# Performance work log

Hardware: AMD Instinct MI355X
Metric: run time of the kernel (lower is better)

## Reference

```python
import jax, jax.numpy as jnp
import numpy as np

WS = 7           # window_size
NUM_HEADS = 4
DIM = 128
BNW = 4096       # batch * num_windows
NW = 64          # windows per image (attn_mask leading dim)
N = WS * WS      # tokens per window = 49


def make_rel_idx(ws: int) -> np.ndarray:
    coords = np.stack(np.meshgrid(np.arange(ws), np.arange(ws), indexing='ij'))  # (2, ws, ws)
    flat = coords.reshape(2, -1)                                                  # (2, N)
    rel = flat[:, :, None] - flat[:, None, :]                                     # (2, N, N)
    rel = rel.transpose(1, 2, 0).copy()
    rel[:, :, 0] += ws - 1
    rel[:, :, 1] += ws - 1
    rel[:, :, 0] *= 2 * ws - 1
    return rel.sum(-1).astype(np.int32)                                           # (N, N)


def setup_inputs() -> dict:
    key = jax.random.key(0)
    ks = jax.random.split(key, 4)
    x = jax.random.normal(ks[0], (BNW, N, DIM), dtype=jnp.float32)
    attn_mask = jnp.zeros((NW, N, N), dtype=jnp.float32)
    qkv_w = jax.random.normal(ks[1], (3 * DIM, DIM), dtype=jnp.float32) * 0.02
    qkv_b = jnp.zeros((3 * DIM,), dtype=jnp.float32)
    proj_w = jax.random.normal(ks[2], (DIM, DIM), dtype=jnp.float32) * 0.02
    proj_b = jnp.zeros((DIM,), dtype=jnp.float32)
    bias_table = jax.random.normal(ks[3], ((2 * WS - 1) ** 2, NUM_HEADS), dtype=jnp.float32) * 0.02
    rel_idx = jnp.asarray(make_rel_idx(WS))
    return {"x": x, "attn_mask": attn_mask, "qkv_w": qkv_w, "qkv_b": qkv_b,
            "proj_w": proj_w, "proj_b": proj_b, "bias_table": bias_table,
            "rel_idx": rel_idx}


def reference(x, attn_mask, qkv_w, qkv_b, proj_w, proj_b, bias_table, rel_idx):
    BnW, n, C = x.shape
    H = NUM_HEADS
    hd = C // H
    scale = hd ** -0.5
    # qkv projection: (BnW, n, 3C) -> (3, BnW, H, n, hd)
    qkv = (x @ qkv_w.T + qkv_b).reshape(BnW, n, 3, H, hd).transpose(2, 0, 3, 1, 4)
    q, k, v = qkv[0], qkv[1], qkv[2]
    attn = jnp.einsum('bhnd,bhmd->bhnm', q * scale, k)          # (BnW, H, n, n)
    bias = bias_table[rel_idx]                                   # (n, n, H)
    attn = attn + bias.transpose(2, 0, 1)[None]                  # broadcast (1, H, n, n)
    nW = attn_mask.shape[0]
    attn = attn.reshape(-1, nW, H, n, n) + attn_mask[None, :, None]
    attn = attn.reshape(-1, H, n, n)
    attn = jax.nn.softmax(attn, axis=-1)
    out = jnp.einsum('bhnm,bhmd->bhnd', attn, v)                 # (BnW, H, n, hd)
    out = out.transpose(0, 2, 1, 3).reshape(BnW, n, C)
    return out @ proj_w.T + proj_b
```

## Files before the change

kernel.cpp:

```cpp
#include <hip/hip_runtime.h>

#define NT   49
#define HD   32
#define NH   4
#define DIM  128
#define SCALEQ 0.17677669529663687f

typedef __attribute__((ext_vector_type(8))) short short8;
typedef __attribute__((ext_vector_type(4))) short short4v;
typedef __attribute__((ext_vector_type(4))) float floatx4;
typedef short8 short8a __attribute__((may_alias));
typedef short4v short4a __attribute__((may_alias));
typedef unsigned long long ulla __attribute__((may_alias));
typedef unsigned long long ull;

__device__ __forceinline__ short f2b(float f) {
    union { float f; unsigned u; } v; v.f = f;
    return (short)((v.u + 0x7fffu + ((v.u >> 16) & 1u)) >> 16);
}
__device__ __forceinline__ float b2f(short s) {
    union { unsigned u; float f; } v; v.u = ((unsigned)(unsigned short)s) << 16;
    return v.f;
}

__global__ __launch_bounds__(256) void wmsa_prep(
        const float* __restrict__ qkvw, const float* __restrict__ projw,
        const float* __restrict__ btab, const int* __restrict__ ridx,
        const float* __restrict__ mask,
        short* __restrict__ wqkv, short* __restrict__ wproj,
        short* __restrict__ cmb) {
    __shared__ __align__(16) int   s_ridx[NT * NT];
    __shared__ __align__(16) float s_btab[169 * 4];
    __shared__ __align__(16) float s_mask[NT * NT];

    const int wdw = blockIdx.x;
    const int tid = threadIdx.x;

    {
        int g = wdw * 256 + tid;
        const float* src = (g < 12288) ? (qkvw + g * 4) : (projw + (g - 12288) * 4);
        float4 v = *(const float4*)src;
        float s = (g < 4096) ? SCALEQ : 1.0f;
        ull pk =  (ull)(unsigned short)f2b(v.x * s)
                | ((ull)(unsigned short)f2b(v.y * s) << 16)
                | ((ull)(unsigned short)f2b(v.z * s) << 32)
                | ((ull)(unsigned short)f2b(v.w * s) << 48);
        if (g < 12288) *(ulla*)(wqkv + g * 4) = pk;
        else           *(ulla*)(wproj + (g - 12288) * 4) = pk;
    }

    for (int i = tid; i < NT * NT; i += 256) s_ridx[i] = ridx[i];
    for (int i = tid; i < 169 * 4; i += 256) s_btab[i] = btab[i];
    {
        const float* mw = mask + (size_t)wdw * NT * NT;
        for (int i = tid; i < NT * NT; i += 256) s_mask[i] = mask ? mw[i] : 0.f;
    }
    __syncthreads();

    #pragma unroll
    for (int gi = 0; gi < 4; ++gi) {
        int g = gi * 256 + tid;
        int cc = g & 15, qq = (g >> 4) & 3, tile = g >> 6;
        int it = tile >> 2, jt = tile & 3;
        int col = jt * 16 + cc;
        int rowb = it * 16 + qq * 4;
        if (col >= NT) {
            ull m16 = (unsigned short)f2b(-1e30f);
            ull pk = m16 | (m16 << 16) | (m16 << 32) | (m16 << 48);
            #pragma unroll
            for (int h = 0; h < NH; ++h)
                *(ulla*)(cmb + (((size_t)wdw * NH + h) << 12) + g * 4) = pk;
        } else {
            float bt[4][4], mv[4];
            #pragma unroll
            for (int r = 0; r < 4; ++r) {
                int row = rowb + r;
                if (row >= NT) {
                    bt[r][0] = bt[r][1] = bt[r][2] = bt[r][3] = 0.f;
                    mv[r] = 0.f;
                } else {
                    int ri = s_ridx[row * NT + col];
                    float4 b4 = *(const float4*)(s_btab + ri * 4);
                    bt[r][0] = b4.x; bt[r][1] = b4.y; bt[r][2] = b4.z; bt[r][3] = b4.w;
                    mv[r] = s_mask[row * NT + col];
                }
            }
            #pragma unroll
            for (int h = 0; h < NH; ++h) {
                ull pk =  (ull)(unsigned short)f2b(bt[0][h] + mv[0])
                        | ((ull)(unsigned short)f2b(bt[1][h] + mv[1]) << 16)
                        | ((ull)(unsigned short)f2b(bt[2][h] + mv[2]) << 32)
                        | ((ull)(unsigned short)f2b(bt[3][h] + mv[3]) << 48);
                *(ulla*)(cmb + (((size_t)wdw * NH + h) << 12) + g * 4) = pk;
            }
        }
    }
}

#define RWAVE 12800
#define OSTR  136
#define LDSB  51200

__global__ __launch_bounds__(256, 3) void wmsa_main(
    const float* __restrict__ x,
    const float* __restrict__ qkvb, const float* __restrict__ projb,
    const short* __restrict__ wqkv, const short* __restrict__ wproj,
    const short* __restrict__ cmb, float* __restrict__ out)
{
    __shared__ __align__(16) char pool[LDSB];
    short* lds = (short*)pool;

    const int b    = blockIdx.x;
    const int wdw  = b & 63;
    const int tid  = threadIdx.x;
    const int wave = tid >> 6;
    const int lane = tid & 63;
    const int qq   = lane >> 4;
    const int cc   = lane & 15;
    const int ccl  = cc & 7, cch = cc >> 3, cm3 = cc & 3;

    const int colbase = wave * 32 + cc;
    short8 bfc[4], bfn[4];
    #pragma unroll
    for (int ks = 0; ks < 4; ++ks)
        bfc[ks] = *(const short8a*)(wqkv + colbase * DIM + ks * 32 + qq * 8);
    float biasv[6];
    #pragma unroll
    for (int j = 0; j < 6; ++j)
        biasv[j] = qkvb[(j >> 1) * DIM + colbase + (j & 1) * 16];

    {
        const float* xb = x + (size_t)b * NT * DIM;
        for (int i = tid; i < NT * 32; i += 256) {
            int t = i >> 5, c4 = (i & 31) << 2;
            float4 v = *(const float4*)(xb + t * DIM + c4);
            ull pk =  (ull)(unsigned short)f2b(v.x)
                    | ((ull)(unsigned short)f2b(v.y) << 16)
                    | ((ull)(unsigned short)f2b(v.z) << 32)
                    | ((ull)(unsigned short)f2b(v.w) << 48);
            *(ulla*)(lds + t * 136 + c4) = pk;
        }
        for (int i = tid; i < (64 - NT) * 32; i += 256) {
            int t = NT + (i >> 5), c4 = (i & 31) << 2;
            *(ulla*)(lds + t * 136 + c4) = 0ull;
        }
    }
    __syncthreads();

    short8 af[4][4];
    #pragma unroll
    for (int it = 0; it < 4; ++it)
        #pragma unroll
        for (int ks = 0; ks < 4; ++ks)
            af[it][ks] = *(const short8a*)(lds + (it * 16 + cc) * 136 + ks * 32 + qq * 8);
    __syncthreads();

    short* qw = (short*)(pool + wave * RWAVE);
    short* kw = qw + 2048;
    short* vw = qw + 4096;
    short* pw = qw;

    #pragma unroll
    for (int jt6 = 0; jt6 < 6; ++jt6) {
        const int sec = jt6 >> 1, hlf = jt6 & 1;
        if (jt6 < 5) {
            const int cn = ((jt6 + 1) >> 1) * DIM + colbase + ((jt6 + 1) & 1) * 16;
            #pragma unroll
            for (int ks = 0; ks < 4; ++ks)
                bfn[ks] = *(const short8a*)(wqkv + cn * DIM + ks * 32 + qq * 8);
        }
        float bias = biasv[jt6];
        if (sec == 0) bias *= SCALEQ;
        const floatx4 cinit = {bias, bias, bias, bias};
        #pragma unroll
        for (int it = 0; it < 4; ++it) {
            floatx4 acc = cinit;
            #pragma unroll
            for (int ks = 0; ks < 4; ++ks)
                acc = __builtin_amdgcn_mfma_f32_16x16x32_bf16(af[it][ks], bfc[ks], acc, 0, 0, 0);
            if (sec == 2) {
                int dd = hlf * 16 + cc;
                int t0 = it * 16 + qq * 4;
                ull pk =  (ull)(unsigned short)f2b(acc[0])
                        | ((ull)(unsigned short)f2b(acc[1]) << 16)
                        | ((ull)(unsigned short)f2b(acc[2]) << 32)
                        | ((ull)(unsigned short)f2b(acc[3]) << 48);
                *(ulla*)(vw + dd * 72 + t0) = pk;
            } else {
                short* dst = (sec == 0) ? qw : kw;
                int gb = hlf * 2 + cch;
                #pragma unroll
                for (int r = 0; r < 4; ++r) {
                    int t = it * 16 + qq * 4 + r;
                    dst[t * 32 + ((gb ^ r) << 3) + ccl] = f2b(acc[r]);
                }
            }
        }
        #pragma unroll
        for (int ks = 0; ks < 4; ++ks) bfc[ks] = bfn[ks];
    }

    short4v cm[16];
    {
        const short* cw = cmb + (((size_t)wdw * NH + wave) << 12);
        #pragma unroll
        for (int t16 = 0; t16 < 16; ++t16)
            cm[t16] = *(const short4a*)(cw + t16 * 256 + qq * 64 + cc * 4);
    }
    __asm__ volatile("" ::: "memory");

    {
        short8 qf[4], kf[4];
        #pragma unroll
        for (int t = 0; t < 4; ++t) {
            qf[t] = *(const short8a*)(qw + (t * 16 + cc) * 32 + ((qq ^ cm3) << 3));
            kf[t] = *(const short8a*)(kw + (t * 16 + cc) * 32 + ((qq ^ cm3) << 3));
        }
        #pragma unroll
        for (int it = 0; it < 4; ++it) {
            floatx4 s[4];
            #pragma unroll
            for (int jt = 0; jt < 4; ++jt) {
                short4v cb = cm[it * 4 + jt];
                floatx4 ci = {b2f(cb.x), b2f(cb.y), b2f(cb.z), b2f(cb.w)};
                s[jt] = __builtin_amdgcn_mfma_f32_16x16x32_bf16(qf[it], kf[jt], ci, 0, 0, 0);
            }
            float e[4][4], inv[4];
            #pragma unroll
            for (int r = 0; r < 4; ++r) {
                float sm = 0.f;
                #pragma unroll
                for (int jt = 0; jt < 4; ++jt) {
                    float ee = __expf(s[jt][r]);
                    e[r][jt] = ee;
                    sm += ee;
                }
                #pragma unroll
                for (int d = 1; d < 16; d <<= 1) sm += __shfl_xor(sm, d);
                inv[r] = 1.0f / sm;
            }
            #pragma unroll
            for (int r = 0; r < 4; ++r) {
                int t = it * 16 + qq * 4 + r;
                #pragma unroll
                for (int jt = 0; jt < 4; ++jt) {
                    int g = (jt * 2 + cch) ^ r;
                    pw[t * 64 + (g << 3) + ccl] = f2b(e[r][jt] * inv[r]);
                }
            }
        }
    }
    __asm__ volatile("" ::: "memory");

    floatx4 o[4][2];
    #pragma unroll
    for (int it = 0; it < 4; ++it)
        #pragma unroll
        for (int jv = 0; jv < 2; ++jv)
            o[it][jv] = (floatx4){0.f, 0.f, 0.f, 0.f};
    #pragma unroll
    for (int ks = 0; ks < 2; ++ks) {
        short8 pf[4], vf[2];
        #pragma unroll
        for (int it = 0; it < 4; ++it)
            pf[it] = *(const short8a*)(pw + (it * 16 + cc) * 64 + (((ks * 4 + qq) ^ cm3) << 3));
        #pragma unroll
        for (int jv = 0; jv < 2; ++jv)
            vf[jv] = *(const short8a*)(vw + (jv * 16 + cc) * 72 + ks * 32 + qq * 8);
        #pragma unroll
        for (int it = 0; it < 4; ++it)
            #pragma unroll
            for (int jv = 0; jv < 2; ++jv)
                o[it][jv] = __builtin_amdgcn_mfma_f32_16x16x32_bf16(pf[it], vf[jv], o[it][jv], 0, 0, 0);
    }

    short8 pcur[4], pnxt[4];
    float pbv[8];
    #pragma unroll
    for (int ks = 0; ks < 4; ++ks) {
        pcur[ks] = *(const short8a*)(wproj + cc * DIM + ks * 32 + qq * 8);
        pnxt[ks] = *(const short8a*)(wproj + (16 + cc) * DIM + ks * 32 + qq * 8);
    }
    #pragma unroll
    for (int j = 0; j < 8; ++j) pbv[j] = projb[j * 16 + cc];

    __syncthreads();

    short* ow = (short*)pool;
    #pragma unroll
    for (int it = 0; it < 4; ++it)
        #pragma unroll
        for (int jv = 0; jv < 2; ++jv)
            #pragma unroll
            for (int r = 0; r < 4; ++r) {
                int t = it * 16 + qq * 4 + r;
                ow[t * OSTR + wave * 32 + jv * 16 + cc] = f2b(o[it][jv][r]);
            }
    __syncthreads();

    {
        short8 a2[4];
        #pragma unroll
        for (int ks = 0; ks < 4; ++ks)
            a2[ks] = *(const short8a*)(ow + (wave * 16 + cc) * OSTR + ks * 32 + qq * 8);
        float* outb = out + (size_t)b * NT * DIM;
        #pragma unroll
        for (int jt = 0; jt < 8; ++jt) {
            short8 pfut[4];
            if (jt < 6) {
                int cn = (jt + 2) * 16 + cc;
                #pragma unroll
                for (int ks = 0; ks < 4; ++ks)
                    pfut[ks] = *(const short8a*)(wproj + cn * DIM + ks * 32 + qq * 8);
            }
            float pb = pbv[jt];
            floatx4 acc = {pb, pb, pb, pb};
            #pragma unroll
            for (int ks = 0; ks < 4; ++ks)
                acc = __builtin_amdgcn_mfma_f32_16x16x32_bf16(a2[ks], pcur[ks], acc, 0, 0, 0);
            int col = jt * 16 + cc;
            #pragma unroll
            for (int r = 0; r < 4; ++r) {
                int row = wave * 16 + qq * 4 + r;
                if (row < NT) outb[row * DIM + col] = acc[r];
            }
            #pragma unroll
            for (int ks = 0; ks < 4; ++ks) { pcur[ks] = pnxt[ks]; pnxt[ks] = pfut[ks]; }
        }
    }
}

extern "C" void kernel_launch(void* const* d_in, const int* in_sizes, int n_in,
                              void* d_out, int out_size, void* d_ws, size_t ws_size,
                              hipStream_t stream) {
    const float* x     = (const float*)d_in[0];
    const float* mask  = (const float*)d_in[1];
    const float* qkvw  = (const float*)d_in[2];
    const float* qkvb  = (const float*)d_in[3];
    const float* projw = (const float*)d_in[4];
    const float* projb = (const float*)d_in[5];
    const float* btab  = (const float*)d_in[6];
    const int*   ridx  = (const int*)d_in[7];
    float* outp = (float*)d_out;

    short* wqkv  = (short*)d_ws;
    short* wproj = (short*)((char*)d_ws + 98304);
    short* cmb   = (short*)((char*)d_ws + 131072);

    wmsa_prep<<<64, 256, 0, stream>>>(qkvw, projw, btab, ridx, mask, wqkv, wproj, cmb);
    wmsa_main<<<4096, 256, 0, stream>>>(x, qkvb, projb, wqkv, wproj, cmb, outp);
}
```

Baseline: 312.3 us.

## Defer softmax normalization using ones-column MFMA row sums; hoist bias loads

Stores unnormalized exp scores to LDS and computes each row's sum with an extra MFMA against a ones vector, then divides the PV output afterwards. This removes the per-row cross-lane shuffle reductions and the per-element multiply before the P@V step. It also moves the combined bias/mask loads earlier so they overlap with the QKV projection, and drops the null-mask check. The trade-off is extra MFMAs, higher register pressure from holding the bias values early, and bf16 rounding of unnormalized exps feeding into the sum.

```diff
diff --git a/kernel.cpp b/kernel.cpp
--- a/kernel.cpp
+++ b/kernel.cpp
@@ -53,7 +53,7 @@
     for (int i = tid; i < 169 * 4; i += 256) s_btab[i] = btab[i];
     {
         const float* mw = mask + (size_t)wdw * NT * NT;
-        for (int i = tid; i < NT * NT; i += 256) s_mask[i] = mask ? mw[i] : 0.f;
+        for (int i = tid; i < NT * NT; i += 256) s_mask[i] = mw[i];
     }
     __syncthreads();
 
@@ -159,6 +159,14 @@
     short* kw = qw + 2048;
     short* vw = qw + 4096;
     short* pw = qw;
+
+    short4v cm[16];
+    {
+        const short* cw = cmb + (((size_t)wdw * NH + wave) << 12);
+        #pragma unroll
+        for (int t16 = 0; t16 < 16; ++t16)
+            cm[t16] = *(const short4a*)(cw + t16 * 256 + qq * 64 + cc * 4);
+    }
 
     #pragma unroll
     for (int jt6 = 0; jt6 < 6; ++jt6) {
@@ -200,13 +208,6 @@
         for (int ks = 0; ks < 4; ++ks) bfc[ks] = bfn[ks];
     }
 
-    short4v cm[16];
-    {
-        const short* cw = cmb + (((size_t)wdw * NH + wave) << 12);
-        #pragma unroll
-        for (int t16 = 0; t16 < 16; ++t16)
-            cm[t16] = *(const short4a*)(cw + t16 * 256 + qq * 64 + cc * 4);
-    }
     __asm__ volatile("" ::: "memory");
 
     {
@@ -225,39 +226,29 @@
                 floatx4 ci = {b2f(cb.x), b2f(cb.y), b2f(cb.z), b2f(cb.w)};
                 s[jt] = __builtin_amdgcn_mfma_f32_16x16x32_bf16(qf[it], kf[jt], ci, 0, 0, 0);
             }
-            float e[4][4], inv[4];
-            #pragma unroll
-            for (int r = 0; r < 4; ++r) {
-                float sm = 0.f;
-                #pragma unroll
-                for (int jt = 0; jt < 4; ++jt) {
-                    float ee = __expf(s[jt][r]);
-                    e[r][jt] = ee;
-                    sm += ee;
-                }
-                #pragma unroll
-                for (int d = 1; d < 16; d <<= 1) sm += __shfl_xor(sm, d);
-                inv[r] = 1.0f / sm;
-            }
             #pragma unroll
             for (int r = 0; r < 4; ++r) {
                 int t = it * 16 + qq * 4 + r;
                 #pragma unroll
                 for (int jt = 0; jt < 4; ++jt) {
+                    float ee = __expf(s[jt][r]);
                     int g = (jt * 2 + cch) ^ r;
-                    pw[t * 64 + (g << 3) + ccl] = f2b(e[r][jt] * inv[r]);
+                    pw[t * 64 + (g << 3) + ccl] = f2b(ee);
                 }
             }
         }
     }
     __asm__ volatile("" ::: "memory");
 
-    floatx4 o[4][2];
-    #pragma unroll
-    for (int it = 0; it < 4; ++it)
-        #pragma unroll
-        for (int jv = 0; jv < 2; ++jv)
-            o[it][jv] = (floatx4){0.f, 0.f, 0.f, 0.f};
+    floatx4 o[4][2], ssum[4];
+    #pragma unroll
+    for (int it = 0; it < 4; ++it) {
+        o[it][0] = (floatx4){0.f, 0.f, 0.f, 0.f};
+        o[it][1] = (floatx4){0.f, 0.f, 0.f, 0.f};
+        ssum[it] = (floatx4){0.f, 0.f, 0.f, 0.f};
+    }
+    const short BONE = (short)0x3F80;
+    const short8 onesf = {BONE, BONE, BONE, BONE, BONE, BONE, BONE, BONE};
     #pragma unroll
     for (int ks = 0; ks < 2; ++ks) {
         short8 pf[4], vf[2];
@@ -268,11 +259,20 @@
         for (int jv = 0; jv < 2; ++jv)
             vf[jv] = *(const short8a*)(vw + (jv * 16 + cc) * 72 + ks * 32 + qq * 8);
         #pragma unroll
-        for (int it = 0; it < 4; ++it)
-            #pragma unroll
-            for (int jv = 0; jv < 2; ++jv)
-                o[it][jv] = __builtin_amdgcn_mfma_f32_16x16x32_bf16(pf[it], vf[jv], o[it][jv], 0, 0, 0);
-    }
+        for (int it = 0; it < 4; ++it) {
+            o[it][0] = __builtin_amdgcn_mfma_f32_16x16x32_bf16(pf[it], vf[0], o[it][0], 0, 0, 0);
+            o[it][1] = __builtin_amdgcn_mfma_f32_16x16x32_bf16(pf[it], vf[1], o[it][1], 0, 0, 0);
+            ssum[it] = __builtin_amdgcn_mfma_f32_16x16x32_bf16(pf[it], onesf, ssum[it], 0, 0, 0);
+        }
+    }
+    #pragma unroll
+    for (int it = 0; it < 4; ++it)
+        #pragma unroll
+        for (int r = 0; r < 4; ++r) {
+            float inv = 1.0f / ssum[it][r];
+            o[it][0][r] *= inv;
+            o[it][1][r] *= inv;
+        }
 
     short8 pcur[4], pnxt[4];
     float pbv[8];
```

Result: faster. 300.2 us (-3.9%).
